# Optimization experiments

Hardware: AMD Instinct MI355X
Metric: run time of the kernel (lower is better)

The kernel has to match this reference:

```python
import jax, jax.numpy as jnp
import numpy as np

N_NODES = 100000
N_EDGES = 1600000
IN_F = 128
OUT_F = 32
HEADS = 2
NEG_SLOPE = 0.2  # DGL GATConv default leaky_relu negative slope


def setup_inputs() -> dict:
    key = jax.random.key(0)
    ks = jax.random.split(key, 12)
    x = jax.random.normal(ks[0], (N_NODES, IN_F), dtype=jnp.float32)
    src = jax.random.randint(ks[1], (N_EDGES,), 0, N_NODES, dtype=jnp.int32)
    dst = jax.random.randint(ks[2], (N_EDGES,), 0, N_NODES, dtype=jnp.int32)
    # GATConv params: fc weight [IN_F, HEADS*OUT_F], attn_l/attn_r [HEADS, OUT_F], bias [HEADS*OUT_F]
    s = 1.0 / np.sqrt(IN_F)
    W = jax.random.normal(ks[3], (IN_F, HEADS * OUT_F), dtype=jnp.float32) * s
    attn_l = jax.random.normal(ks[4], (HEADS, OUT_F), dtype=jnp.float32) * s
    attn_r = jax.random.normal(ks[5], (HEADS, OUT_F), dtype=jnp.float32) * s
    bias_gat = jnp.zeros((HEADS * OUT_F,), dtype=jnp.float32)
    # MLPPredictor: lin1 (2*OUT_F -> OUT_F), lin2 (OUT_F -> 1)
    s1 = 1.0 / np.sqrt(2 * OUT_F)
    W1 = jax.random.normal(ks[6], (2 * OUT_F, OUT_F), dtype=jnp.float32) * s1
    b1 = jnp.zeros((OUT_F,), dtype=jnp.float32)
    s2 = 1.0 / np.sqrt(OUT_F)
    W2 = jax.random.normal(ks[7], (OUT_F, 1), dtype=jnp.float32) * s2
    b2 = jnp.zeros((1,), dtype=jnp.float32)
    return {"x": x, "W": W, "attn_l": attn_l, "attn_r": attn_r,
            "bias_gat": bias_gat, "W1": W1, "b1": b1, "W2": W2, "b2": b2,
            "src": src, "dst": dst}


def _forward(x, W, attn_l, attn_r, bias_gat, W1, b1, W2, b2, src, dst):
    # --- GATConv(in, out, 2 heads) ---
    feat = (x @ W).reshape(N_NODES, HEADS, OUT_F)           # [N,H,F]
    el = jnp.einsum('nhf,hf->nh', feat, attn_l)             # [N,H]
    er = jnp.einsum('nhf,hf->nh', feat, attn_r)             # [N,H]
    e = jax.nn.leaky_relu(el[src] + er[dst], NEG_SLOPE)     # [E,H]
    # edge softmax over incoming edges of each dst node (numerically stable)
    m = jax.ops.segment_max(e, dst, num_segments=N_NODES)   # [N,H]
    ex = jnp.exp(e - m[dst])                                # [E,H]
    denom = jax.ops.segment_sum(ex, dst, num_segments=N_NODES)  # [N,H]
    alpha = ex / denom[dst]                                 # [E,H]
    msg = feat[src] * alpha[:, :, None]                     # [E,H,F]
    rst = jax.ops.segment_sum(msg, dst, num_segments=N_NODES)   # [N,H,F]
    rst = rst + bias_gat.reshape(HEADS, OUT_F)
    h = jax.nn.relu(jnp.mean(rst, axis=1))                  # [N,F]
    # --- MLPPredictor: per-edge concat(src,dst) -> lin1 -> lin2 (no activation) ---
    hcat = jnp.concatenate([h[src], h[dst]], axis=1)        # [E,2F]
    score = (hcat @ W1 + b1) @ W2 + b2                      # [E,1]
    return score


def reference(x, W, attn_l, attn_r, bias_gat, W1, b1, W2, b2, src, dst):
    return _forward(x, W, attn_l, attn_r, bias_gat, W1, b1, W2, b2, src, dst)
```

## Files before the change

kernel.cpp:

```cpp
#include <hip/hip_runtime.h>
#include <hip/hip_fp16.h>

#define N_NODES 100000
#define N_EDGES 1600000
#define IN_F 128
#define OUT_F 32
#define HEADS 2
#define HO 64

#define NBUCK 782
#define BIN_BLOCKS 400
#define BIN_THREADS 512
#define EPB (N_EDGES / BIN_BLOCKS)
#define CAP 28
#define LCAP 2368

__global__ void feat_k(const float* __restrict__ x, const float* __restrict__ W,
                       const float* __restrict__ attn_l, const float* __restrict__ attn_r,
                       __half* __restrict__ feat16, float* __restrict__ el, float* __restrict__ er,
                       const float* __restrict__ W1, const float* __restrict__ b1,
                       const float* __restrict__ W2, const float* __restrict__ b2,
                       float* __restrict__ wcomb, float* __restrict__ ccomb){
  __shared__ __align__(16) float Ws[IN_F*HO];
  __shared__ __align__(16) float xs[64*132];
  int tid = threadIdx.x;
  if (blockIdx.x == 0){
    if (tid < HO){
      float a = 0.f;
      for (int k = 0; k < OUT_F; ++k) a = fmaf(W1[tid*OUT_F + k], W2[k], a);
      wcomb[tid] = a;
    }
    if (tid == HO){
      float a = 0.f;
      for (int k = 0; k < OUT_F; ++k) a = fmaf(b1[k], W2[k], a);
      *ccomb = a + b2[0];
    }
  }
  int node0 = blockIdx.x*64;
  for (int i = tid; i < 2048; i += 256)
    ((float4*)Ws)[i] = ((const float4*)W)[i];
  for (int i = tid; i < 2048; i += 256){
    int ln = i >> 5, kq = i & 31;
    int n = node0 + ln;
    float4 v = (n < N_NODES) ? ((const float4*)x)[(size_t)n*32 + kq]
                             : make_float4(0.f,0.f,0.f,0.f);
    *(float4*)&xs[ln*132 + kq*4] = v;
  }
  __syncthreads();

  int nq = tid >> 4, cq = tid & 15;
  int n0 = nq*4, c0 = cq*4;
  float acc[4][4] = {{0.f,0.f,0.f,0.f},{0.f,0.f,0.f,0.f},{0.f,0.f,0.f,0.f},{0.f,0.f,0.f,0.f}};

  for (int k = 0; k < IN_F; k += 4){
    float xk[4][4];
    #pragma unroll
    for (int j = 0; j < 4; ++j){
      float4 t = *(const float4*)&xs[(n0+j)*132 + k];
      xk[j][0]=t.x; xk[j][1]=t.y; xk[j][2]=t.z; xk[j][3]=t.w;
    }
    #pragma unroll
    for (int d = 0; d < 4; ++d){
      float4 w4 = *(const float4*)&Ws[(k+d)*HO + c0];
      #pragma unroll
      for (int j = 0; j < 4; ++j){
        acc[j][0] = fmaf(xk[j][d], w4.x, acc[j][0]);
        acc[j][1] = fmaf(xk[j][d], w4.y, acc[j][1]);
        acc[j][2] = fmaf(xk[j][d], w4.z, acc[j][2]);
        acc[j][3] = fmaf(xk[j][d], w4.w, acc[j][3]);
      }
    }
  }

  float4 al4 = *(const float4*)&attn_l[c0];
  float4 ar4 = *(const float4*)&attn_r[c0];
  #pragma unroll
  for (int j = 0; j < 4; ++j){
    int n = node0 + n0 + j;
    float p = acc[j][0]*al4.x + acc[j][1]*al4.y + acc[j][2]*al4.z + acc[j][3]*al4.w;
    float q = acc[j][0]*ar4.x + acc[j][1]*ar4.y + acc[j][2]*ar4.z + acc[j][3]*ar4.w;
    #pragma unroll
    for (int off = 4; off; off >>= 1){ p += __shfl_xor(p, off); q += __shfl_xor(q, off); }
    if (n < N_NODES){
      __half2 h01 = __float22half2_rn(make_float2(acc[j][0], acc[j][1]));
      __half2 h23 = __float22half2_rn(make_float2(acc[j][2], acc[j][3]));
      union { uint2 u; __half2 h[2]; } pk; pk.h[0]=h01; pk.h[1]=h23;
      *(uint2*)&feat16[(size_t)n*HO + c0] = pk.u;
      if ((cq & 7) == 0){
        int h = cq >> 3;
        el[n*HEADS + h] = p;
        er[n*HEADS + h] = q;
      }
    }
  }
}

__global__ void bin_k(const int* __restrict__ src, const int* __restrict__ dst,
                      const float* __restrict__ el, const float* __restrict__ er,
                      int* __restrict__ counts, uint2* __restrict__ stg){
  __shared__ int cnt[NBUCK];
  int tid = threadIdx.x, blk = blockIdx.x;
  for (int i = tid; i < NBUCK; i += BIN_THREADS) cnt[i] = 0;
  __syncthreads();
  const int4* s4p = (const int4*)(src + blk*EPB);
  const int4* d4p = (const int4*)(dst + blk*EPB);
  for (int i = tid; i < EPB/4; i += BIN_THREADS){
    int4 s4 = s4p[i];
    int4 d4 = d4p[i];
    int ss[4] = {s4.x, s4.y, s4.z, s4.w};
    int dd[4] = {d4.x, d4.y, d4.z, d4.w};
    #pragma unroll
    for (int u = 0; u < 4; ++u){
      int s = ss[u], d = dd[u];
      float2 elv = *(const float2*)&el[s*HEADS];
      float2 erv = *(const float2*)&er[d*HEADS];
      float t0 = elv.x + erv.x, t1 = elv.y + erv.y;
      t0 = t0 > 0.f ? t0 : 0.2f*t0;
      t1 = t1 > 0.f ? t1 : 0.2f*t1;
      __half2 ex2 = __float22half2_rn(make_float2(__expf(t0), __expf(t1)));
      int b = d >> 7;
      int slot = atomicAdd(&cnt[b], 1);
      if (slot < CAP)
        stg[((size_t)blk*NBUCK + b)*CAP + slot] =
          make_uint2(((unsigned int)s << 7) | (unsigned int)(d & 127),
                     *(const unsigned int*)&ex2);
    }
  }
  __syncthreads();
  for (int i = tid; i < NBUCK; i += BIN_THREADS)
    counts[blk*NBUCK + i] = cnt[i] < CAP ? cnt[i] : CAP;
}

__global__ void __launch_bounds__(512, 8) scatter_agg_k(
                              const int* __restrict__ counts, const uint2* __restrict__ stg,
                              const __half* __restrict__ feat16, const float* __restrict__ bias,
                              const float* __restrict__ wcomb,
                              float* __restrict__ s1, float* __restrict__ s2){
  __shared__ uint2 lsev_raw[LCAP];
  __shared__ uint2 lsev[LCAP];
  __shared__ int hist[128];
  __shared__ int start[128];
  __shared__ int cur[128];
  __shared__ int wtot[2];
  __shared__ int ltotal;
  int b = blockIdx.x;
  int tid = threadIdx.x;
  int w = tid >> 6, lane = tid & 63;
  if (tid < 128) hist[tid] = 0;
  if (tid == 0) ltotal = 0;
  __syncthreads();

  int grp = tid >> 3, gl = tid & 7;
  for (int blk = grp; blk < BIN_BLOCKS; blk += 64){
    int n = counts[blk*NBUCK + b];
    int base = 0;
    if (gl == 0 && n) base = atomicAdd(&ltotal, n);
    base = __shfl(base, (lane & 56));
    const uint2* seg = stg + ((size_t)blk*NBUCK + b)*CAP;
    for (int j = gl; j < n; j += 8){
      uint2 r = seg[j];
      atomicAdd(&hist[r.x & 127], 1);
      if (base + j < LCAP) lsev_raw[base + j] = r;
    }
  }
  __syncthreads();

  int v = 0, inc = 0;
  if (tid < 128){
    v = hist[tid];
    inc = v;
    #pragma unroll
    for (int off = 1; off < 64; off <<= 1){
      int t = __shfl_up(inc, off);
      if (lane >= off) inc += t;
    }
    if (lane == 63) wtot[w] = inc;
  }
  __syncthreads();
  if (tid == 0){ int t0 = wtot[0]; wtot[0] = 0; wtot[1] = t0; }
  __syncthreads();
  if (tid < 128){
    int excl = wtot[w] + inc - v;
    start[tid] = excl;
    cur[tid] = excl;
  }
  __syncthreads();

  int tot = ltotal < LCAP ? ltotal : LCAP;
  for (int i = tid; i < tot; i += 512){
    uint2 r = lsev_raw[i];
    int pos = atomicAdd(&cur[r.x & 127], 1);
    lsev[pos] = make_uint2(r.x >> 7, r.y);
  }
  __syncthreads();

  int g  = lane >> 4;
  int c4 = lane & 15;
  int h  = (c4 >= 8);
  float b0v = bias[c4*4 + 0], b1v = bias[c4*4 + 1], b2v = bias[c4*4 + 2], b3v = bias[c4*4 + 3];
  int f0 = (c4 & 7)*4;
  float w0 = wcomb[f0], w1 = wcomb[f0+1], w2 = wcomb[f0+2], w3 = wcomb[f0+3];
  float u0 = wcomb[32+f0], u1 = wcomb[32+f0+1], u2 = wcomb[32+f0+2], u3 = wcomb[32+f0+3];
  for (int i = 0; i < 16; ++i){
    int nl = w*16 + i;
    int node = (b << 7) + nl;
    if (node >= N_NODES) break;
    int s0 = start[nl];
    int deg = cur[nl] - s0;

    float sum0 = 0.f, sum1 = 0.f;
    for (int jj = lane; jj < deg; jj += 64){
      unsigned int u = lsev[s0 + jj].y;
      float2 e = __half22float2(*(const __half2*)&u);
      sum0 += e.x; sum1 += e.y;
    }
    #pragma unroll
    for (int off = 32; off; off >>= 1){
      sum0 += __shfl_xor(sum0, off);
      sum1 += __shfl_xor(sum1, off);
    }
    float r0 = sum0 > 0.f ? 1.f/sum0 : 0.f;
    float r1 = sum1 > 0.f ? 1.f/sum1 : 0.f;
    float rh = h ? r1 : r0;

    float a0=0.f, a1=0.f, a2=0.f, a3=0.f;
    for (int j0 = 0; j0 < deg; j0 += 8){
      int ja = j0 + g, jb = j0 + 4 + g;
      float alA = 0.f, alB = 0.f;
      int snA = 0, snB = 0;
      if (ja < deg){
        uint2 r = lsev[s0 + ja];
        snA = r.x;
        float2 e = __half22float2(*(const __half2*)&r.y);
        alA = (h ? e.y : e.x) * rh;
      }
      if (jb < deg){
        uint2 r = lsev[s0 + jb];
        snB = r.x;
        float2 e = __half22float2(*(const __half2*)&r.y);
        alB = (h ? e.y : e.x) * rh;
      }
      uint2 vA = *(const uint2*)(feat16 + (size_t)snA*HO + c4*4);
      uint2 vB = *(const uint2*)(feat16 + (size_t)snB*HO + c4*4);
      float2 fA01 = __half22float2(*(const __half2*)&vA.x);
      float2 fA23 = __half22float2(*(const __half2*)&vA.y);
      float2 fB01 = __half22float2(*(const __half2*)&vB.x);
      float2 fB23 = __half22float2(*(const __half2*)&vB.y);
      a0 = fmaf(alA, fA01.x, a0); a0 = fmaf(alB, fB01.x, a0);
      a1 = fmaf(alA, fA01.y, a1); a1 = fmaf(alB, fB01.y, a1);
      a2 = fmaf(alA, fA23.x, a2); a2 = fmaf(alB, fB23.x, a2);
      a3 = fmaf(alA, fA23.y, a3); a3 = fmaf(alB, fB23.y, a3);
    }
    a0 += __shfl_xor(a0, 16); a1 += __shfl_xor(a1, 16); a2 += __shfl_xor(a2, 16); a3 += __shfl_xor(a3, 16);
    a0 += __shfl_xor(a0, 32); a1 += __shfl_xor(a1, 32); a2 += __shfl_xor(a2, 32); a3 += __shfl_xor(a3, 32);
    a0 += b0v; a1 += b1v; a2 += b2v; a3 += b3v;
    float h0 = 0.5f*(a0 + __shfl_xor(a0, 8)); h0 = fmaxf(h0, 0.f);
    float h1 = 0.5f*(a1 + __shfl_xor(a1, 8)); h1 = fmaxf(h1, 0.f);
    float h2 = 0.5f*(a2 + __shfl_xor(a2, 8)); h2 = fmaxf(h2, 0.f);
    float h3 = 0.5f*(a3 + __shfl_xor(a3, 8)); h3 = fmaxf(h3, 0.f);
    float p = h0*w0 + h1*w1 + h2*w2 + h3*w3;
    float q = h0*u0 + h1*u1 + h2*u2 + h3*u3;
    #pragma unroll
    for (int off = 4; off; off >>= 1){
      p += __shfl_xor(p, off);
      q += __shfl_xor(q, off);
    }
    if (lane == 0){ s1[node] = p; s2[node] = q; }
  }
}

__global__ void edge_score_k(const int* __restrict__ src, const int* __restrict__ dst,
                             const float* __restrict__ s1, const float* __restrict__ s2,
                             const float* __restrict__ ccomb, float* __restrict__ out){
  int i = blockIdx.x*blockDim.x + threadIdx.x;
  if (i >= N_EDGES/4) return;
  int4 s4 = ((const int4*)src)[i];
  int4 d4 = ((const int4*)dst)[i];
  float c = ccomb[0];
  float4 o;
  o.x = s1[s4.x] + s2[d4.x] + c;
  o.y = s1[s4.y] + s2[d4.y] + c;
  o.z = s1[s4.z] + s2[d4.z] + c;
  o.w = s1[s4.w] + s2[d4.w] + c;
  ((float4*)out)[i] = o;
}

extern "C" void kernel_launch(void* const* d_in, const int* in_sizes, int n_in,
                              void* d_out, int out_size, void* d_ws, size_t ws_size,
                              hipStream_t stream){
  const float* x      = (const float*)d_in[0];
  const float* W      = (const float*)d_in[1];
  const float* attn_l = (const float*)d_in[2];
  const float* attn_r = (const float*)d_in[3];
  const float* bias   = (const float*)d_in[4];
  const float* W1     = (const float*)d_in[5];
  const float* b1     = (const float*)d_in[6];
  const float* W2     = (const float*)d_in[7];
  const float* b2     = (const float*)d_in[8];
  const int*   src    = (const int*)d_in[9];
  const int*   dst    = (const int*)d_in[10];
  float* out = (float*)d_out;

  float* ws = (float*)d_ws;
  size_t off = 0;
  __half* feat16 = (__half*)(ws + off); off += (size_t)N_NODES*HO/2;
  float*  el     = ws + off; off += (size_t)N_NODES*HEADS;
  float*  er     = ws + off; off += (size_t)N_NODES*HEADS;
  float*  s1     = ws + off; off += N_NODES;
  float*  s2     = ws + off; off += N_NODES;
  float*  wcomb  = ws + off; off += 64;
  float*  ccomb  = ws + off; off += 64;
  int*    counts = (int*)(ws + off); off += (size_t)BIN_BLOCKS*NBUCK;
  off = (off + 1) & ~(size_t)1;
  uint2*  stg    = (uint2*)(ws + off); off += (size_t)2*BIN_BLOCKS*NBUCK*CAP;

  feat_k<<<(N_NODES + 63)/64, 256, 0, stream>>>(x, W, attn_l, attn_r, feat16, el, er,
                                                W1, b1, W2, b2, wcomb, ccomb);
  bin_k<<<BIN_BLOCKS, BIN_THREADS, 0, stream>>>(src, dst, el, er, counts, stg);
  scatter_agg_k<<<NBUCK, 512, 0, stream>>>(counts, stg, feat16, bias, wcomb, s1, s2);
  edge_score_k<<<(N_EDGES/4 + 255)/256, 256, 0, stream>>>(src, dst, s1, s2, ccomb, out);
}
```

Baseline: 269.0 us.

## Fuse softmax denominator into binning, widen gather unroll, resize bin blocks

Runs the binning stage with fewer, larger blocks (200×1024 threads) and a larger per-bucket capacity. It accumulates per-destination softmax denominators with shared-memory float atomics while loading staged edges, which removes the separate per-node reduction pass over the local edge list. It also unrolls the feature gather loop to four edges per lane group to keep more loads in flight. Shared float atomics add contention, make the summation order nondeterministic, and the staging buffer grows with the larger CAP.

Result: faster. 259.7 us (-3.5%).

```diff
diff --git a/kernel.cpp b/kernel.cpp
--- a/kernel.cpp
+++ b/kernel.cpp
@@ -9,10 +9,10 @@
 #define HO 64
 
 #define NBUCK 782
-#define BIN_BLOCKS 400
-#define BIN_THREADS 512
+#define BIN_BLOCKS 200
+#define BIN_THREADS 1024
 #define EPB (N_EDGES / BIN_BLOCKS)
-#define CAP 28
+#define CAP 36
 #define LCAP 2368
 
 __global__ void feat_k(const float* __restrict__ x, const float* __restrict__ W,
@@ -141,12 +141,14 @@
   __shared__ int hist[128];
   __shared__ int start[128];
   __shared__ int cur[128];
+  __shared__ float dsum[256];
   __shared__ int wtot[2];
   __shared__ int ltotal;
   int b = blockIdx.x;
   int tid = threadIdx.x;
   int w = tid >> 6, lane = tid & 63;
   if (tid < 128) hist[tid] = 0;
+  if (tid < 256) dsum[tid] = 0.f;
   if (tid == 0) ltotal = 0;
   __syncthreads();
 
@@ -159,7 +161,11 @@
     const uint2* seg = stg + ((size_t)blk*NBUCK + b)*CAP;
     for (int j = gl; j < n; j += 8){
       uint2 r = seg[j];
-      atomicAdd(&hist[r.x & 127], 1);
+      int dl = r.x & 127;
+      atomicAdd(&hist[dl], 1);
+      float2 e = __half22float2(*(const __half2*)&r.y);
+      atomicAdd(&dsum[dl], e.x);
+      atomicAdd(&dsum[128 + dl], e.y);
       if (base + j < LCAP) lsev_raw[base + j] = r;
     }
   }
@@ -207,49 +213,42 @@
     if (node >= N_NODES) break;
     int s0 = start[nl];
     int deg = cur[nl] - s0;
-
-    float sum0 = 0.f, sum1 = 0.f;
-    for (int jj = lane; jj < deg; jj += 64){
-      unsigned int u = lsev[s0 + jj].y;
-      float2 e = __half22float2(*(const __half2*)&u);
-      sum0 += e.x; sum1 += e.y;
-    }
-    #pragma unroll
-    for (int off = 32; off; off >>= 1){
-      sum0 += __shfl_xor(sum0, off);
-      sum1 += __shfl_xor(sum1, off);
-    }
-    float r0 = sum0 > 0.f ? 1.f/sum0 : 0.f;
-    float r1 = sum1 > 0.f ? 1.f/sum1 : 0.f;
-    float rh = h ? r1 : r0;
+    float sh = h ? dsum[128 + nl] : dsum[nl];
+    float rh = sh > 0.f ? 1.f/sh : 0.f;
 
     float a0=0.f, a1=0.f, a2=0.f, a3=0.f;
-    for (int j0 = 0; j0 < deg; j0 += 8){
-      int ja = j0 + g, jb = j0 + 4 + g;
-      float alA = 0.f, alB = 0.f;
-      int snA = 0, snB = 0;
-      if (ja < deg){
-        uint2 r = lsev[s0 + ja];
-        snA = r.x;
-        float2 e = __half22float2(*(const __half2*)&r.y);
-        alA = (h ? e.y : e.x) * rh;
-      }
-      if (jb < deg){
-        uint2 r = lsev[s0 + jb];
-        snB = r.x;
-        float2 e = __half22float2(*(const __half2*)&r.y);
-        alB = (h ? e.y : e.x) * rh;
-      }
+    for (int j0 = 0; j0 < deg; j0 += 16){
+      int jA = j0 + g, jB = j0 + 4 + g, jC = j0 + 8 + g, jD = j0 + 12 + g;
+      float alA=0.f, alB=0.f, alC=0.f, alD=0.f;
+      int snA=0, snB=0, snC=0, snD=0;
+      if (jA < deg){ uint2 r = lsev[s0+jA]; snA = r.x;
+        float2 e = __half22float2(*(const __half2*)&r.y); alA = (h?e.y:e.x)*rh; }
+      if (jB < deg){ uint2 r = lsev[s0+jB]; snB = r.x;
+        float2 e = __half22float2(*(const __half2*)&r.y); alB = (h?e.y:e.x)*rh; }
+      if (jC < deg){ uint2 r = lsev[s0+jC]; snC = r.x;
+        float2 e = __half22float2(*(const __half2*)&r.y); alC = (h?e.y:e.x)*rh; }
+      if (jD < deg){ uint2 r = lsev[s0+jD]; snD = r.x;
+        float2 e = __half22float2(*(const __half2*)&r.y); alD = (h?e.y:e.x)*rh; }
       uint2 vA = *(const uint2*)(feat16 + (size_t)snA*HO + c4*4);
       uint2 vB = *(const uint2*)(feat16 + (size_t)snB*HO + c4*4);
+      uint2 vC = *(const uint2*)(feat16 + (size_t)snC*HO + c4*4);
+      uint2 vD = *(const uint2*)(feat16 + (size_t)snD*HO + c4*4);
       float2 fA01 = __half22float2(*(const __half2*)&vA.x);
       float2 fA23 = __half22float2(*(const __half2*)&vA.y);
       float2 fB01 = __half22float2(*(const __half2*)&vB.x);
       float2 fB23 = __half22float2(*(const __half2*)&vB.y);
+      float2 fC01 = __half22float2(*(const __half2*)&vC.x);
+      float2 fC23 = __half22float2(*(const __half2*)&vC.y);
+      float2 fD01 = __half22float2(*(const __half2*)&vD.x);
+      float2 fD23 = __half22float2(*(const __half2*)&vD.y);
       a0 = fmaf(alA, fA01.x, a0); a0 = fmaf(alB, fB01.x, a0);
+      a0 = fmaf(alC, fC01.x, a0); a0 = fmaf(alD, fD01.x, a0);
       a1 = fmaf(alA, fA01.y, a1); a1 = fmaf(alB, fB01.y, a1);
+      a1 = fmaf(alC, fC01.y, a1); a1 = fmaf(alD, fD01.y, a1);
       a2 = fmaf(alA, fA23.x, a2); a2 = fmaf(alB, fB23.x, a2);
+      a2 = fmaf(alC, fC23.x, a2); a2 = fmaf(alD, fD23.x, a2);
       a3 = fmaf(alA, fA23.y, a3); a3 = fmaf(alB, fB23.y, a3);
+      a3 = fmaf(alC, fC23.y, a3); a3 = fmaf(alD, fD23.y, a3);
     }
     a0 += __shfl_xor(a0, 16); a1 += __shfl_xor(a1, 16); a2 += __shfl_xor(a2, 16); a3 += __shfl_xor(a3, 16);
     a0 += __shfl_xor(a0, 32); a1 += __shfl_xor(a1, 32); a2 += __shfl_xor(a2, 32); a3 += __shfl_xor(a3, 32);
```
